# Kernel optimization log

Measured on AMD Instinct MI355X. Metric: run time of the kernel, lower is better.

## Reference

```python
import jax, jax.numpy as jnp
import numpy as np

SPARSITY = 0.01

def quantize(weight, s):
    # ternary quantization: (-s, 0, +s); computed under no_grad in torch
    pos = (weight > s).astype(weight.dtype)
    neg = (weight < -s).astype(weight.dtype)
    return (pos - neg) * s

def setup_inputs() -> dict:
    key = jax.random.key(0)
    k1, k2, k3 = jax.random.split(key, 3)
    B, N, Din, Dout = 8, 2048, 256, 256
    x = jax.random.normal(k1, (B, N, Din), dtype=jnp.float32)
    adj = jax.random.uniform(k2, (B, N, N), dtype=jnp.float32)
    # xavier_uniform_ over (in_dim, out_dim)
    limit = float(np.sqrt(6.0 / (Din + Dout)))
    weight = jax.random.uniform(k3, (Din, Dout), dtype=jnp.float32, minval=-limit, maxval=limit)
    bias = jnp.zeros((Dout,), dtype=jnp.float32)
    return {"x": x, "adj": adj, "weight": weight, "bias": bias}

def reference(x, adj, weight, bias):
    dw = quantize(weight, SPARSITY)          # [Din, Dout] ternary * s
    support = jnp.einsum('bni,io->bno', x, dw)   # [B, N, Dout]
    out = jnp.einsum('bnm,bmo->bno', adj, support) + bias
    return jax.nn.relu(out)
```

## Files before the change

kernel.cpp:

```cpp
#include <hip/hip_runtime.h>
#include <stdint.h>

typedef __attribute__((ext_vector_type(8))) short short8;
typedef __attribute__((ext_vector_type(4))) float f32x4;

static_assert(sizeof(short8) == 16, "frag size");

__device__ __forceinline__ uint16_t f2bf(float f) {
  uint32_t u = __builtin_bit_cast(uint32_t, f);
  u += 0x7fffu + ((u >> 16) & 1u);
  return (uint16_t)(u >> 16);
}

__device__ __forceinline__ void gload_lds16(const void* g, void* lds_wave_base) {
  __builtin_amdgcn_global_load_lds(
      (__attribute__((address_space(1))) void*)(void*)(g),
      (__attribute__((address_space(3))) void*)(lds_wave_base),
      16, 0, 0);
}


__global__ __launch_bounds__(256) void quant_kernel(const float* __restrict__ w,
                                                    uint16_t* __restrict__ dwT) {
  const int o = blockIdx.x, i = threadIdx.x;
  const float v = w[i * 256 + o];
  const float t = (v > 0.01f) ? 1.0f : ((v < -0.01f) ? -1.0f : 0.0f);
  dwT[o * 256 + (i ^ ((o & 7) << 3))] = f2bf(t);
}

__global__ __launch_bounds__(256) void adjcvt_kernel(const float* __restrict__ adj,
                                                     uint16_t* __restrict__ adjB) {
  const int g = blockIdx.x;
  const int c = threadIdx.x;
  const float* p = adj + (size_t)g * 2048 + c * 8;
  const float4 v0 = *(const float4*)p;
  const float4 v1 = *(const float4*)(p + 4);
  uint4 u;
  u.x = (uint32_t)f2bf(v0.x) | ((uint32_t)f2bf(v0.y) << 16);
  u.y = (uint32_t)f2bf(v0.z) | ((uint32_t)f2bf(v0.w) << 16);
  u.z = (uint32_t)f2bf(v1.x) | ((uint32_t)f2bf(v1.y) << 16);
  u.w = (uint32_t)f2bf(v1.z) | ((uint32_t)f2bf(v1.w) << 16);
  const int phys = (c & ~7) | ((c & 7) ^ (g & 7));
  *(uint4*)(adjB + (size_t)g * 2048 + phys * 8) = u;
}

#define SB_A 0
#define SB_B 16384

__global__ __launch_bounds__(256) void support_kernel(const float* __restrict__ x,
                                                      const uint16_t* __restrict__ dwT,
                                                      uint16_t* __restrict__ spt) {
  __shared__ __align__(16) unsigned char smem[24576];
  const int t = threadIdx.x, lane = t & 63, w = t >> 6;
  const int r = lane & 15, q = lane >> 4;
  const int g0 = (blockIdx.x & 127) * 128;
  const int o0 = (blockIdx.x >> 7) * 64;

  f32x4 acc[2][4] = {};

  for (int k0 = 0; k0 < 256; k0 += 64) {
#pragma unroll
    for (int it = 0; it < 4; ++it) {
      const int id = it * 256 + t, row = id >> 3, c = id & 7;
      const float* p = x + (size_t)(g0 + row) * 256 + k0 + c * 8;
      const float4 v0 = *(const float4*)p;
      const float4 v1 = *(const float4*)(p + 4);
      uint4 u;
      u.x = (uint32_t)f2bf(v0.x) | ((uint32_t)f2bf(v0.y) << 16);
      u.y = (uint32_t)f2bf(v0.z) | ((uint32_t)f2bf(v0.w) << 16);
      u.z = (uint32_t)f2bf(v1.x) | ((uint32_t)f2bf(v1.y) << 16);
      u.w = (uint32_t)f2bf(v1.z) | ((uint32_t)f2bf(v1.w) << 16);
      *(uint4*)(smem + SB_A + row * 128 + ((c ^ (row & 7)) << 4)) = u;
    }
#pragma unroll
    for (int j = 0; j < 2; ++j) {
      const int id = j * 256 + t, row = id >> 3, c = id & 7;
      gload_lds16(dwT + (size_t)(o0 + row) * 256 + k0 + c * 8,
                  smem + SB_B + (size_t)(j * 256 + w * 64) * 16);
    }
    __syncthreads();
#pragma unroll
    for (int h = 0; h < 2; ++h) {
      short8 av[2], bv[4];
      const int pc = (((h * 4 + q) ^ (r & 7)) << 4);
#pragma unroll
      for (int mi = 0; mi < 2; ++mi)
        av[mi] = *(const short8*)(smem + SB_A + (32 * w + 16 * mi + r) * 128 + pc);
#pragma unroll
      for (int ni = 0; ni < 4; ++ni)
        bv[ni] = *(const short8*)(smem + SB_B + (16 * ni + r) * 128 + pc);
#pragma unroll
      for (int mi = 0; mi < 2; ++mi)
#pragma unroll
        for (int ni = 0; ni < 4; ++ni)
          acc[mi][ni] = __builtin_amdgcn_mfma_f32_16x16x32_bf16(av[mi], bv[ni],
                                                                acc[mi][ni], 0, 0, 0);
    }
    __syncthreads();
  }
#pragma unroll
  for (int ni = 0; ni < 4; ++ni) {
    const int ol = 16 * ni + r;
#pragma unroll
    for (int mi = 0; mi < 2; ++mi)
#pragma unroll
      for (int reg = 0; reg < 4; ++reg) {
        const int gl = 32 * w + 16 * mi + 4 * q + reg;
        const int gsw = gl ^ ((ol & 7) << 3);
        *(uint16_t*)(smem + (ol * 128 + gsw) * 2) = f2bf(acc[mi][ni][reg] * 0.01f);
      }
  }
  __syncthreads();
#pragma unroll
  for (int it = 0; it < 4; ++it) {
    const int id = it * 256 + t, row = id >> 4, cc = id & 15;
    const uint4 u = *(const uint4*)(smem + (row * 128 + cc * 8) * 2);
    *(uint4*)(spt + (size_t)(o0 + row) * 16384 + g0 + cc * 8) = u;
  }
}

#define MB_A 0
#define MB_B 16384

__global__ __launch_bounds__(256) void gcn_main_kernel(const uint16_t* __restrict__ adjB,
                                                       const uint16_t* __restrict__ spt,
                                                       const float* __restrict__ bias,
                                                       float* __restrict__ out) {
  __shared__ __align__(16) unsigned char smem[24576];
  const int t = threadIdx.x, lane = t & 63, w = t >> 6;
  const int r = lane & 15, q = lane >> 4;
  const int bb = blockIdx.x & 7;
  const int n0 = ((blockIdx.x >> 3) & 15) * 128;
  const int o0 = (blockIdx.x >> 7) * 64;
  const uint16_t* adjb = adjB + ((size_t)bb * 2048 + n0) * 2048;
  const uint16_t* sptb = spt + (size_t)bb * 2048;

  f32x4 acc[2][4] = {};

  for (int k0 = 0; k0 < 2048; k0 += 64) {
#pragma unroll
    for (int j = 0; j < 4; ++j) {
      const int id = j * 256 + t, row = id >> 3, c = id & 7;
      gload_lds16(adjb + (size_t)row * 2048 + k0 + c * 8,
                  smem + MB_A + (size_t)(j * 256 + w * 64) * 16);
    }
#pragma unroll
    for (int j = 0; j < 2; ++j) {
      const int id = j * 256 + t, row = id >> 3, c = id & 7;
      gload_lds16(sptb + (size_t)(o0 + row) * 16384 + k0 + c * 8,
                  smem + MB_B + (size_t)(j * 256 + w * 64) * 16);
    }
    __syncthreads();
#pragma unroll
    for (int h = 0; h < 2; ++h) {
      short8 av[2], bv[4];
      const int pc = (((h * 4 + q) ^ (r & 7)) << 4);
#pragma unroll
      for (int mi = 0; mi < 2; ++mi)
        av[mi] = *(const short8*)(smem + MB_A + (32 * w + 16 * mi + r) * 128 + pc);
#pragma unroll
      for (int ni = 0; ni < 4; ++ni)
        bv[ni] = *(const short8*)(smem + MB_B + (16 * ni + r) * 128 + pc);
#pragma unroll
      for (int mi = 0; mi < 2; ++mi)
#pragma unroll
        for (int ni = 0; ni < 4; ++ni)
          acc[mi][ni] = __builtin_amdgcn_mfma_f32_16x16x32_bf16(av[mi], bv[ni],
                                                                acc[mi][ni], 0, 0, 0);
    }
    __syncthreads();
  }
#pragma unroll
  for (int ni = 0; ni < 4; ++ni) {
    const int o = o0 + 16 * ni + r;
    const float bs = bias[o];
#pragma unroll
    for (int mi = 0; mi < 2; ++mi)
#pragma unroll
      for (int reg = 0; reg < 4; ++reg) {
        const int n = n0 + 32 * w + 16 * mi + 4 * q + reg;
        out[((size_t)bb * 2048 + n) * 256 + o] = fmaxf(acc[mi][ni][reg] + bs, 0.0f);
      }
  }
}

extern "C" void kernel_launch(void* const* d_in, const int* in_sizes, int n_in,
                              void* d_out, int out_size, void* d_ws, size_t ws_size,
                              hipStream_t stream) {
  const float* x      = (const float*)d_in[0];
  const float* adj    = (const float*)d_in[1];
  const float* weight = (const float*)d_in[2];
  const float* bias   = (const float*)d_in[3];
  float* out = (float*)d_out;

  uint16_t* dwT  = (uint16_t*)d_ws;
  uint16_t* spt  = (uint16_t*)((char*)d_ws + (131072));
  uint16_t* adjB = (uint16_t*)((char*)d_ws + (131072 + 8388608));

  hipLaunchKernelGGL(quant_kernel,    dim3(256),   dim3(256), 0, stream, weight, dwT);
  hipLaunchKernelGGL(adjcvt_kernel,   dim3(16384), dim3(256), 0, stream, adj, adjB);
  hipLaunchKernelGGL(support_kernel,  dim3(512),   dim3(256), 0, stream, x, dwT, spt);
  hipLaunchKernelGGL(gcn_main_kernel, dim3(512),   dim3(256), 0, stream, adjB, spt, bias, out);
}
```

Baseline: 255.2 us.

## Fuse adj bf16 conversion into main GEMM and retile to full output width

Removes the separate adj-to-bf16 conversion kernel and its 64MB intermediate. The main kernel now loads fp32 adj directly, converts it in registers and stores it swizzled into LDS. It also retiles so each block covers 32 rows by all 256 output columns, which means adj is read exactly once and the whole support slice is streamed per k-step. The cost is synchronous fp32 loads for A (no async global-to-LDS path), 8 support loads per step and a larger LDS footprint.

```diff
diff --git a/kernel.cpp b/kernel.cpp
--- a/kernel.cpp
+++ b/kernel.cpp
@@ -26,22 +26,6 @@
   const float v = w[i * 256 + o];
   const float t = (v > 0.01f) ? 1.0f : ((v < -0.01f) ? -1.0f : 0.0f);
   dwT[o * 256 + (i ^ ((o & 7) << 3))] = f2bf(t);
-}
-
-__global__ __launch_bounds__(256) void adjcvt_kernel(const float* __restrict__ adj,
-                                                     uint16_t* __restrict__ adjB) {
-  const int g = blockIdx.x;
-  const int c = threadIdx.x;
-  const float* p = adj + (size_t)g * 2048 + c * 8;
-  const float4 v0 = *(const float4*)p;
-  const float4 v1 = *(const float4*)(p + 4);
-  uint4 u;
-  u.x = (uint32_t)f2bf(v0.x) | ((uint32_t)f2bf(v0.y) << 16);
-  u.y = (uint32_t)f2bf(v0.z) | ((uint32_t)f2bf(v0.w) << 16);
-  u.z = (uint32_t)f2bf(v1.x) | ((uint32_t)f2bf(v1.y) << 16);
-  u.w = (uint32_t)f2bf(v1.z) | ((uint32_t)f2bf(v1.w) << 16);
-  const int phys = (c & ~7) | ((c & 7) ^ (g & 7));
-  *(uint4*)(adjB + (size_t)g * 2048 + phys * 8) = u;
 }
 
 #define SB_A 0
@@ -120,34 +104,39 @@
 }
 
 #define MB_A 0
-#define MB_B 16384
+#define MB_B 4096
 
-__global__ __launch_bounds__(256) void gcn_main_kernel(const uint16_t* __restrict__ adjB,
+__global__ __launch_bounds__(256) void gcn_main_kernel(const float* __restrict__ adj,
                                                        const uint16_t* __restrict__ spt,
                                                        const float* __restrict__ bias,
                                                        float* __restrict__ out) {
-  __shared__ __align__(16) unsigned char smem[24576];
+  __shared__ __align__(16) unsigned char smem[36864];
   const int t = threadIdx.x, lane = t & 63, w = t >> 6;
   const int r = lane & 15, q = lane >> 4;
   const int bb = blockIdx.x & 7;
-  const int n0 = ((blockIdx.x >> 3) & 15) * 128;
-  const int o0 = (blockIdx.x >> 7) * 64;
-  const uint16_t* adjb = adjB + ((size_t)bb * 2048 + n0) * 2048;
+  const int n0 = (blockIdx.x >> 3) * 32;
+  const float* adjb = adj + ((size_t)bb * 2048 + n0) * 2048;
   const uint16_t* sptb = spt + (size_t)bb * 2048;
 
   f32x4 acc[2][4] = {};
 
   for (int k0 = 0; k0 < 2048; k0 += 64) {
-#pragma unroll
-    for (int j = 0; j < 4; ++j) {
-      const int id = j * 256 + t, row = id >> 3, c = id & 7;
-      gload_lds16(adjb + (size_t)row * 2048 + k0 + c * 8,
-                  smem + MB_A + (size_t)(j * 256 + w * 64) * 16);
+    {
+      const int row = t >> 3, c = t & 7;
+      const float* p = adjb + (size_t)row * 2048 + k0 + c * 8;
+      const float4 v0 = *(const float4*)p;
+      const float4 v1 = *(const float4*)(p + 4);
+      uint4 u;
+      u.x = (uint32_t)f2bf(v0.x) | ((uint32_t)f2bf(v0.y) << 16);
+      u.y = (uint32_t)f2bf(v0.z) | ((uint32_t)f2bf(v0.w) << 16);
+      u.z = (uint32_t)f2bf(v1.x) | ((uint32_t)f2bf(v1.y) << 16);
+      u.w = (uint32_t)f2bf(v1.z) | ((uint32_t)f2bf(v1.w) << 16);
+      *(uint4*)(smem + MB_A + row * 128 + ((c ^ (row & 7)) << 4)) = u;
     }
 #pragma unroll
-    for (int j = 0; j < 2; ++j) {
+    for (int j = 0; j < 8; ++j) {
       const int id = j * 256 + t, row = id >> 3, c = id & 7;
-      gload_lds16(sptb + (size_t)(o0 + row) * 16384 + k0 + c * 8,
+      gload_lds16(sptb + (size_t)row * 16384 + k0 + c * 8,
                   smem + MB_B + (size_t)(j * 256 + w * 64) * 16);
     }
     __syncthreads();
@@ -157,10 +146,10 @@
       const int pc = (((h * 4 + q) ^ (r & 7)) << 4);
 #pragma unroll
       for (int mi = 0; mi < 2; ++mi)
-        av[mi] = *(const short8*)(smem + MB_A + (32 * w + 16 * mi + r) * 128 + pc);
+        av[mi] = *(const short8*)(smem + MB_A + (16 * mi + r) * 128 + pc);
 #pragma unroll
       for (int ni = 0; ni < 4; ++ni)
-        bv[ni] = *(const short8*)(smem + MB_B + (16 * ni + r) * 128 + pc);
+        bv[ni] = *(const short8*)(smem + MB_B + (w * 64 + 16 * ni + r) * 128 + pc);
 #pragma unroll
       for (int mi = 0; mi < 2; ++mi)
 #pragma unroll
@@ -172,13 +161,13 @@
   }
 #pragma unroll
   for (int ni = 0; ni < 4; ++ni) {
-    const int o = o0 + 16 * ni + r;
+    const int o = w * 64 + 16 * ni + r;
     const float bs = bias[o];
 #pragma unroll
     for (int mi = 0; mi < 2; ++mi)
 #pragma unroll
       for (int reg = 0; reg < 4; ++reg) {
-        const int n = n0 + 32 * w + 16 * mi + 4 * q + reg;
+        const int n = n0 + 16 * mi + 4 * q + reg;
         out[((size_t)bb * 2048 + n) * 256 + o] = fmaxf(acc[mi][ni][reg] + bs, 0.0f);
       }
   }
@@ -193,12 +182,10 @@
   const float* bias   = (const float*)d_in[3];
   float* out = (float*)d_out;
 
-  uint16_t* dwT  = (uint16_t*)d_ws;
-  uint16_t* spt  = (uint16_t*)((char*)d_ws + (131072));
-  uint16_t* adjB = (uint16_t*)((char*)d_ws + (131072 + 8388608));
+  uint16_t* dwT = (uint16_t*)d_ws;
+  uint16_t* spt = (uint16_t*)((char*)d_ws + 131072);
 
-  hipLaunchKernelGGL(quant_kernel,    dim3(256),   dim3(256), 0, stream, weight, dwT);
-  hipLaunchKernelGGL(adjcvt_kernel,   dim3(16384), dim3(256), 0, stream, adj, adjB);
-  hipLaunchKernelGGL(support_kernel,  dim3(512),   dim3(256), 0, stream, x, dwT, spt);
-  hipLaunchKernelGGL(gcn_main_kernel, dim3(512),   dim3(256), 0, stream, adjB, spt, bias, out);
+  hipLaunchKernelGGL(quant_kernel,    dim3(256), dim3(256), 0, stream, weight, dwT);
+  hipLaunchKernelGGL(support_kernel,  dim3(512), dim3(256), 0, stream, x, dwT, spt);
+  hipLaunchKernelGGL(gcn_main_kernel, dim3(512), dim3(256), 0, stream, adj, spt, bias, out);
 }
```

Result: faster. 236.3 us (-7.4%).
